# Kernel tuning notes

Measured on AMD Instinct MI355X. Metric: run time of the kernel, lower is better.

The kernel has to match this reference:

```python
import jax, jax.numpy as jnp
import numpy as np

B, DM, H, M, K = 2, 256, 4, 4096, 16
DIM = DM // H  # per-head feature dim = 64


def _proj(x, W, b):
    # 1x1 Conv2d on channels-first (B, C, M, K): pointwise linear over channels
    return jnp.einsum('oi,bimk->bomk', W, x) + b[None, :, None, None]


def setup_inputs() -> dict:
    rng = jax.random.key(0)
    ks = jax.random.split(rng, 11)
    s = 1.0 / np.sqrt(DM)
    return {
        'query': jax.random.normal(ks[0], (B, DM, M, 1), jnp.float32),
        'key':   jax.random.normal(ks[1], (B, DM, M, K), jnp.float32),
        'value': jax.random.normal(ks[2], (B, DM, M, K), jnp.float32),
        'Wq': jax.random.normal(ks[3], (DM, DM), jnp.float32) * s,
        'bq': jax.random.normal(ks[4], (DM,), jnp.float32) * 0.01,
        'Wk': jax.random.normal(ks[5], (DM, DM), jnp.float32) * s,
        'bk': jax.random.normal(ks[6], (DM,), jnp.float32) * 0.01,
        'Wv': jax.random.normal(ks[7], (DM, DM), jnp.float32) * s,
        'bv': jax.random.normal(ks[8], (DM,), jnp.float32) * 0.01,
        'Wm': jax.random.normal(ks[9], (DM, DM), jnp.float32) * s,
        'bm': jax.random.normal(ks[10], (DM,), jnp.float32) * 0.01,
    }


def reference(query, key, value, Wq, bq, Wk, bk, Wv, bv, Wm, bm):
    # project; torch view(B, dim, heads, -1) on channels-first => channel c -> (d=c//H, h=c%H)
    q = _proj(query, Wq, bq).reshape(B, DIM, H, M)          # (b, d, h, m)
    k = _proj(key,   Wk, bk).reshape(B, DIM, H, M, K)        # (b, d, h, m, k)
    v = _proj(value, Wv, bv).reshape(B, DIM, H, M, K)
    scores = jnp.einsum('bfhm,bfhmk->bhmk', q, k) / np.sqrt(DIM).astype(np.float32)
    prob = jax.nn.softmax(scores, axis=-1)                   # softmax over kn neighbors
    x = jnp.einsum('bhmk,bdhmk->bdhm', prob, v)              # (b, d, h, m)
    out = _proj(x.reshape(B, DM, M, 1), Wm, bm)              # merge 1x1 conv
    prob_sum = jnp.sum(prob, axis=1)                         # (b, m, k)
    return out, prob_sum
```

## Files before the change

kernel.cpp:

```cpp
#include <hip/hip_runtime.h>
#include <stdint.h>

#define DM_ 256
#define H_ 4
#define M_ 4096
#define KN_ 16
#define B_ 2
#define MK_ (M_*KN_)

typedef __attribute__((ext_vector_type(8))) short short8;
typedef __attribute__((ext_vector_type(4))) float f32x4;
typedef __attribute__((ext_vector_type(4))) unsigned short u16x4;

static __device__ __forceinline__ unsigned short f2bf(float x) {
  union { float f; uint32_t u; } v; v.f = x;
  uint32_t u = v.u + (0x7FFFu + ((v.u >> 16) & 1u));
  return (unsigned short)(u >> 16);
}
static __device__ __forceinline__ float u2f(uint32_t u) {
  union { uint32_t u; float f; } v; v.u = u; return v.f;
}

static __device__ __forceinline__ int swz512(int col, int kbyte) {
  int f = ((col >> 2) & 7) ^ ((col & 1) << 2);
  return (col << 9) + (kbyte ^ (f << 4));
}

__global__ void prep2(const float* __restrict__ Wq, const float* __restrict__ bq,
                      const float* __restrict__ Wk, const float* __restrict__ Wv,
                      const float* __restrict__ bv, const float* __restrict__ Wm,
                      const float* __restrict__ bm,
                      unsigned short* __restrict__ W2T, unsigned short* __restrict__ Wmv,
                      float* __restrict__ qb2, float* __restrict__ btot) {
  int t = blockIdx.x * 512 + threadIdx.x;
  if (t < 262144) {
    int j = t & 7, lane = (t >> 3) & 63, rowblk = (t >> 9) & 63, kstep = t >> 15;
    int row = rowblk * 16 + (lane & 15);
    int k = kstep * 32 + (lane >> 4) * 8 + j;
    int h = row >> 8, c = row & 255;
    float v = 0.f;
#pragma unroll 8
    for (int d = 0; d < 64; ++d) v += Wq[(4 * d + h) * 256 + k] * Wk[(4 * d + h) * 256 + c];
    W2T[t] = f2bf(v);
  } else if (t < 524288) {
    int e = t - 262144;
    int j = e & 7, lane = (e >> 3) & 63, rowblk = (e >> 9) & 15, kstep = e >> 13;
    int o = rowblk * 16 + (lane & 15);
    int kidx = kstep * 32 + (lane >> 4) * 8 + j;
    int c = kidx >> 2, h = kidx & 3;
    float v = 0.f;
#pragma unroll 8
    for (int d = 0; d < 64; ++d) v += Wm[o * 256 + 4 * d + h] * Wv[(4 * d + h) * 256 + c];
    Wmv[e] = f2bf(v);
  } else if (t < 525312) {
    int r = t - 524288; int h = r >> 8, c = r & 255;
    float v = 0.f;
#pragma unroll 8
    for (int d = 0; d < 64; ++d) v += bq[4 * d + h] * Wk[(4 * d + h) * 256 + c];
    qb2[r] = v;
  } else if (t < 525568) {
    int o = t - 525312;
    float v = bm[o];
#pragma unroll 8
    for (int c2 = 0; c2 < 256; ++c2) v += Wm[o * 256 + c2] * bv[c2];
    btot[o] = v;
  }
}

__global__ __launch_bounds__(512)
void qw_gemm(const float* __restrict__ query, const unsigned short* __restrict__ W2T,
             const float* __restrict__ qb2, unsigned short* __restrict__ qWbuf) {
  __shared__ unsigned short Xl[32 * 256];
  const int tid = threadIdx.x;
  const int lane = tid & 63, wid = tid >> 6;
  const int wr = wid >> 1, wc = wid & 1;
  const int mt = blockIdx.x & 127;
  const int rt = (blockIdx.x >> 7) & 3;
  const int b = blockIdx.x >> 9;
  const int m0 = mt * 32;
  const float* Xb = query + (size_t)b * DM_ * M_ + m0;
  const int c4 = 4 * (tid & 7);
  const int ch0 = 4 * (tid >> 3);
  float4 f[4];
#pragma unroll
  for (int i = 0; i < 4; ++i) f[i] = *(const float4*)(Xb + (size_t)(ch0 + i) * M_ + c4);
#pragma unroll
  for (int j = 0; j < 4; ++j) {
    u16x4 u = { f2bf(((const float*)&f[0])[j]), f2bf(((const float*)&f[1])[j]),
                f2bf(((const float*)&f[2])[j]), f2bf(((const float*)&f[3])[j]) };
    *(u16x4*)((char*)Xl + swz512(c4 + j, 2 * ch0)) = u;
  }
  __syncthreads();
  f32x4 acc[4] = {};
  const int bcol = wc * 16 + (lane & 15);
  const int rdk = 16 * (lane >> 4);
  short8 a_cur[4], a_nxt[4];
#pragma unroll
  for (int fi = 0; fi < 4; ++fi)
    a_cur[fi] = *(const short8*)(W2T + (size_t)(((rt * 16 + wr * 4 + fi) * 64 + lane) * 8));
#pragma unroll
  for (int kgs = 0; kgs < 8; ++kgs) {
    if (kgs < 7) {
#pragma unroll
      for (int fi = 0; fi < 4; ++fi)
        a_nxt[fi] = *(const short8*)(W2T + (size_t)((((kgs + 1) * 64 + rt * 16 + wr * 4 + fi) * 64 + lane) * 8));
    }
    short8 bb = *(const short8*)((const char*)Xl + swz512(bcol, 64 * kgs + rdk));
#pragma unroll
    for (int fi = 0; fi < 4; ++fi)
      acc[fi] = __builtin_amdgcn_mfma_f32_16x16x32_bf16(a_cur[fi], bb, acc[fi], 0, 0, 0);
#pragma unroll
    for (int fi = 0; fi < 4; ++fi) a_cur[fi] = a_nxt[fi];
  }
#pragma unroll
  for (int fi = 0; fi < 4; ++fi) {
#pragma unroll
    for (int r = 0; r < 4; ++r) {
      const int rr = rt * 256 + wr * 64 + fi * 16 + (lane >> 4) * 4 + r;
      qWbuf[(size_t)(b * 1024 + rr) * M_ + m0 + bcol] = f2bf(acc[fi][r] + qb2[rr]);
    }
  }
}

__global__ __launch_bounds__(1024, 8)
void fused_attn(const float* __restrict__ key, const float* __restrict__ value,
                const unsigned short* __restrict__ qW, const unsigned short* __restrict__ Wmv,
                const float* __restrict__ btot, float* __restrict__ out,
                float* __restrict__ psum) {
  __shared__ float ldsA[16 * 64 * 17];
  __shared__ float ldsP[16 * 4 * 16];
  unsigned short* qsl = (unsigned short*)ldsA;
  const int tid = threadIdx.x;
  const int lane = tid & 63;
  const int w = tid >> 6;
  const int vb = (blockIdx.x & 7) * 64 + (blockIdx.x >> 3);
  const int b = vb >> 8;
  const int m0 = (vb & 255) * 16;
  {
    const int c = tid & 255, h = tid >> 8;
    const unsigned short* src = qW + ((size_t)(b * 1024 + h * 256 + c)) * M_ + m0;
    uint4 rv[2];
    rv[0] = *(const uint4*)(src);
    rv[1] = *(const uint4*)(src + 8);
    const unsigned short* rs = (const unsigned short*)rv;
#pragma unroll
    for (int q = 0; q < 16; ++q) {
      const int slot = (q + c) & 15;
      qsl[c * 64 + slot * 4 + h] = rs[q];
    }
  }
  __syncthreads();
  const int mp = lane >> 2;
  const int kkq = lane & 3;
  const size_t cbase = (size_t)(b * 256) * 65536 + (size_t)m0 * 16 + lane * 4;
  f32x4 ps0 = {}, ps1 = {}, ps2 = {}, ps3 = {};
#pragma unroll 4
  for (int i = 0; i < 16; ++i) {
    const int c = i * 16 + w;
    const f32x4 kv = *(const f32x4*)(key + cbase + (size_t)c * 65536);
    const int slot = (mp + c) & 15;
    const uint2 qv = *(const uint2*)&qsl[c * 64 + slot * 4];
    ps0 += kv * u2f(qv.x << 16);
    ps1 += kv * u2f(qv.x & 0xffff0000u);
    ps2 += kv * u2f(qv.y << 16);
    ps3 += kv * u2f(qv.y & 0xffff0000u);
  }
  __syncthreads();
  {
    float* scx = ldsA + w * 1088 + lane * 17;
#pragma unroll
    for (int j = 0; j < 4; ++j) {
      scx[j]      = ps0[j];
      scx[4 + j]  = ps1[j];
      scx[8 + j]  = ps2[j];
      scx[12 + j] = ps3[j];
    }
  }
  __syncthreads();
  {
    const int mp2 = tid >> 6;
    const int h2 = (lane >> 4) & 3;
    const int kk = lane & 15;
    const int lanep = mp2 * 4 + (kk >> 2);
    const int idx = h2 * 4 + (kk & 3);
    float sc = 0.f;
#pragma unroll
    for (int w2 = 0; w2 < 16; ++w2) sc += ldsA[w2 * 1088 + lanep * 17 + idx];
    sc *= 0.125f;
    float mx = sc;
    mx = fmaxf(mx, __shfl_xor(mx, 1)); mx = fmaxf(mx, __shfl_xor(mx, 2));
    mx = fmaxf(mx, __shfl_xor(mx, 4)); mx = fmaxf(mx, __shfl_xor(mx, 8));
    const float e = __expf(sc - mx);
    float sm = e;
    sm += __shfl_xor(sm, 1); sm += __shfl_xor(sm, 2);
    sm += __shfl_xor(sm, 4); sm += __shfl_xor(sm, 8);
    const float pb = e / sm;
    ldsP[(mp2 * 4 + h2) * 16 + kk] = pb;
    float tot = pb;
    tot += __shfl_xor(tot, 16); tot += __shfl_xor(tot, 32);
    if (lane < 16)
      psum[((size_t)b * M_ + m0 + mp2) * KN_ + kk] = tot;
  }
  __syncthreads();
  {
    const f32x4 pr0 = *(const f32x4*)&ldsP[(mp * 4 + 0) * 16 + kkq * 4];
    const f32x4 pr1 = *(const f32x4*)&ldsP[(mp * 4 + 1) * 16 + kkq * 4];
    const f32x4 pr2 = *(const f32x4*)&ldsP[(mp * 4 + 2) * 16 + kkq * 4];
    const f32x4 pr3 = *(const f32x4*)&ldsP[(mp * 4 + 3) * 16 + kkq * 4];
#pragma unroll 4
    for (int i = 0; i < 16; ++i) {
      const int c = i * 16 + w;
      const f32x4 vv = *(const f32x4*)(value + cbase + (size_t)c * 65536);
      float p0 = pr0[0] * vv[0] + pr0[1] * vv[1] + pr0[2] * vv[2] + pr0[3] * vv[3];
      float p1 = pr1[0] * vv[0] + pr1[1] * vv[1] + pr1[2] * vv[2] + pr1[3] * vv[3];
      float p2 = pr2[0] * vv[0] + pr2[1] * vv[1] + pr2[2] * vv[2] + pr2[3] * vv[3];
      float p3 = pr3[0] * vv[0] + pr3[1] * vv[1] + pr3[2] * vv[2] + pr3[3] * vv[3];
      p0 += __shfl_xor(p0, 1); p0 += __shfl_xor(p0, 2);
      p1 += __shfl_xor(p1, 1); p1 += __shfl_xor(p1, 2);
      p2 += __shfl_xor(p2, 1); p2 += __shfl_xor(p2, 2);
      p3 += __shfl_xor(p3, 1); p3 += __shfl_xor(p3, 2);
      if (kkq == 0) {
        uint2 o;
        o.x = (uint32_t)f2bf(p0) | ((uint32_t)f2bf(p1) << 16);
        o.y = (uint32_t)f2bf(p2) | ((uint32_t)f2bf(p3) << 16);
        *(uint2*)((char*)ldsA + ((mp * 2048 + c * 8) ^ ((mp & 7) << 4))) = o;
      }
    }
  }
  __syncthreads();
  {
    const int wid = tid >> 6;
    const int bcol = lane & 15;
    const int kgrp = lane >> 4;
    f32x4 acc = {};
    for (int kgs = 0; kgs < 32; ++kgs) {
      const int byte = (bcol * 2048 + kgs * 64 + kgrp * 16) ^ ((bcol & 7) << 4);
      const short8 bb = *(const short8*)((const char*)ldsA + byte);
      const short8 a0 = *(const short8*)(Wmv + (size_t)(((kgs * 16 + wid) * 64 + lane) * 8));
      acc = __builtin_amdgcn_mfma_f32_16x16x32_bf16(a0, bb, acc, 0, 0, 0);
    }
#pragma unroll
    for (int r = 0; r < 4; ++r) {
      const int o = wid * 16 + kgrp * 4 + r;
      out[((size_t)(b * DM_ + o)) * M_ + m0 + bcol] = acc[r] + btot[o];
    }
  }
}

extern "C" void kernel_launch(void* const* d_in, const int* in_sizes, int n_in,
                              void* d_out, int out_size, void* d_ws, size_t ws_size,
                              hipStream_t stream) {
  const float* query = (const float*)d_in[0];
  const float* key   = (const float*)d_in[1];
  const float* value = (const float*)d_in[2];
  const float* Wq = (const float*)d_in[3];
  const float* bq = (const float*)d_in[4];
  const float* Wk = (const float*)d_in[5];
  const float* bk = (const float*)d_in[6];  (void)bk;
  const float* Wv = (const float*)d_in[7];
  const float* bv = (const float*)d_in[8];
  const float* Wm = (const float*)d_in[9];
  const float* bm = (const float*)d_in[10];
  float* out  = (float*)d_out;
  float* psum = out + (size_t)B_ * DM_ * M_;

  const size_t Wmv_off  = 524288;
  const size_t qb2_off  = 1048576;
  const size_t btot_off = 1052672;
  const size_t qW_off   = 1053696;

  unsigned short* W2T   = (unsigned short*)d_ws;
  unsigned short* Wmv   = (unsigned short*)((char*)d_ws + Wmv_off);
  float* qb2            = (float*)((char*)d_ws + qb2_off);
  float* btot           = (float*)((char*)d_ws + btot_off);
  unsigned short* qWbuf = (unsigned short*)((char*)d_ws + qW_off);

  prep2<<<dim3(1027), dim3(512), 0, stream>>>(Wq, bq, Wk, Wv, bv, Wm, bm, W2T, Wmv, qb2, btot);
  qw_gemm<<<dim3(B_ * 4 * 128), dim3(512), 0, stream>>>(query, W2T, qb2, qWbuf);
  fused_attn<<<dim3(512), dim3(1024), 0, stream>>>(key, value, qWbuf, Wmv, btot, out, psum);
}
```

Before: 103.3 us.

## Double-buffer key/value streaming via async global-to-LDS loads

Replaces direct per-thread global loads of key and value with global_load_lds DMA into a double-buffered LDS staging area. Each loop step issues the next 32-channel chunk before computing on the current one, with explicit vmcnt waits and barriers. The aim is to overlap memory latency with score and PV compute. The cost is a 100KB LDS footprint, which limits the kernel to one 1024-thread block per CU, plus extra block-wide barriers in every iteration.

```diff
diff --git a/kernel.cpp b/kernel.cpp
--- a/kernel.cpp
+++ b/kernel.cpp
@@ -122,14 +122,15 @@
   }
 }
 
-__global__ __launch_bounds__(1024, 8)
+__global__ __launch_bounds__(1024, 4)
 void fused_attn(const float* __restrict__ key, const float* __restrict__ value,
                 const unsigned short* __restrict__ qW, const unsigned short* __restrict__ Wmv,
                 const float* __restrict__ btot, float* __restrict__ out,
                 float* __restrict__ psum) {
-  __shared__ float ldsA[16 * 64 * 17];
-  __shared__ float ldsP[16 * 4 * 16];
-  unsigned short* qsl = (unsigned short*)ldsA;
+  __shared__ __align__(16) char LDS[102400];
+  unsigned short* qsl = (unsigned short*)(LDS + 65536);
+  float* scxp = (float*)LDS;
+  float* ldsP = (float*)(LDS + 98304);
   const int tid = threadIdx.x;
   const int lane = tid & 63;
   const int w = tid >> 6;
@@ -152,22 +153,54 @@
   __syncthreads();
   const int mp = lane >> 2;
   const int kkq = lane & 3;
-  const size_t cbase = (size_t)(b * 256) * 65536 + (size_t)m0 * 16 + lane * 4;
+  const float* ksrc = key   + (size_t)(b * 256) * 65536 + (size_t)m0 * 16 + lane * 4;
+  const float* vsrc = value + (size_t)(b * 256) * 65536 + (size_t)m0 * 16 + lane * 4;
+  auto issue2 = [&](const float* src, int i) {
+    const int h = i & 1;
+#pragma unroll
+    for (int j = 0; j < 2; ++j) {
+      const int r = w * 2 + j;
+      __builtin_amdgcn_global_load_lds(
+          (const __attribute__((address_space(1))) uint32_t*)(src + (size_t)(i * 32 + r) * 65536),
+          (__attribute__((address_space(3))) uint32_t*)(LDS + h * 32768 + r * 1024),
+          16, 0, 0);
+    }
+  };
   f32x4 ps0 = {}, ps1 = {}, ps2 = {}, ps3 = {};
-#pragma unroll 4
-  for (int i = 0; i < 16; ++i) {
-    const int c = i * 16 + w;
-    const f32x4 kv = *(const f32x4*)(key + cbase + (size_t)c * 65536);
-    const int slot = (mp + c) & 15;
-    const uint2 qv = *(const uint2*)&qsl[c * 64 + slot * 4];
-    ps0 += kv * u2f(qv.x << 16);
-    ps1 += kv * u2f(qv.x & 0xffff0000u);
-    ps2 += kv * u2f(qv.y << 16);
-    ps3 += kv * u2f(qv.y & 0xffff0000u);
-  }
+  auto scoreChunk = [&](int i) {
+    const int h = i & 1;
+#pragma unroll
+    for (int j = 0; j < 2; ++j) {
+      const int r = w * 2 + j;
+      const int c = i * 32 + r;
+      const f32x4 kv = *(const f32x4*)(LDS + h * 32768 + r * 1024 + lane * 16);
+      const int slot = (mp + c) & 15;
+      const uint2 qv = *(const uint2*)&qsl[c * 64 + slot * 4];
+      ps0 += kv * u2f(qv.x << 16);
+      ps1 += kv * u2f(qv.x & 0xffff0000u);
+      ps2 += kv * u2f(qv.y << 16);
+      ps3 += kv * u2f(qv.y & 0xffff0000u);
+    }
+  };
+  issue2(ksrc, 0);
+#pragma unroll 1
+  for (int i = 0; i < 7; ++i) {
+    issue2(ksrc, i + 1);
+    __builtin_amdgcn_sched_barrier(0);
+    asm volatile("s_waitcnt vmcnt(2)" ::: "memory");
+    __builtin_amdgcn_sched_barrier(0);
+    __builtin_amdgcn_s_barrier();
+    scoreChunk(i);
+    __builtin_amdgcn_s_barrier();
+    asm volatile("" ::: "memory");
+  }
+  asm volatile("s_waitcnt vmcnt(0)" ::: "memory");
+  __builtin_amdgcn_sched_barrier(0);
+  __builtin_amdgcn_s_barrier();
+  scoreChunk(7);
   __syncthreads();
   {
-    float* scx = ldsA + w * 1088 + lane * 17;
+    float* scx = scxp + w * 1088 + lane * 17;
 #pragma unroll
     for (int j = 0; j < 4; ++j) {
       scx[j]      = ps0[j];
@@ -185,7 +218,7 @@
     const int idx = h2 * 4 + (kk & 3);
     float sc = 0.f;
 #pragma unroll
-    for (int w2 = 0; w2 < 16; ++w2) sc += ldsA[w2 * 1088 + lanep * 17 + idx];
+    for (int w2 = 0; w2 < 16; ++w2) sc += scxp[w2 * 1088 + lanep * 17 + idx];
     sc *= 0.125f;
     float mx = sc;
     mx = fmaxf(mx, __shfl_xor(mx, 1)); mx = fmaxf(mx, __shfl_xor(mx, 2));
@@ -202,15 +235,17 @@
       psum[((size_t)b * M_ + m0 + mp2) * KN_ + kk] = tot;
   }
   __syncthreads();
-  {
-    const f32x4 pr0 = *(const f32x4*)&ldsP[(mp * 4 + 0) * 16 + kkq * 4];
-    const f32x4 pr1 = *(const f32x4*)&ldsP[(mp * 4 + 1) * 16 + kkq * 4];
-    const f32x4 pr2 = *(const f32x4*)&ldsP[(mp * 4 + 2) * 16 + kkq * 4];
-    const f32x4 pr3 = *(const f32x4*)&ldsP[(mp * 4 + 3) * 16 + kkq * 4];
-#pragma unroll 4
-    for (int i = 0; i < 16; ++i) {
-      const int c = i * 16 + w;
-      const f32x4 vv = *(const f32x4*)(value + cbase + (size_t)c * 65536);
+  const f32x4 pr0 = *(const f32x4*)&ldsP[(mp * 4 + 0) * 16 + kkq * 4];
+  const f32x4 pr1 = *(const f32x4*)&ldsP[(mp * 4 + 1) * 16 + kkq * 4];
+  const f32x4 pr2 = *(const f32x4*)&ldsP[(mp * 4 + 2) * 16 + kkq * 4];
+  const f32x4 pr3 = *(const f32x4*)&ldsP[(mp * 4 + 3) * 16 + kkq * 4];
+  auto pvChunk = [&](int i) {
+    const int h = i & 1;
+#pragma unroll
+    for (int j = 0; j < 2; ++j) {
+      const int r = w * 2 + j;
+      const int c = i * 32 + r;
+      const f32x4 vv = *(const f32x4*)(LDS + h * 32768 + r * 1024 + lane * 16);
       float p0 = pr0[0] * vv[0] + pr0[1] * vv[1] + pr0[2] * vv[2] + pr0[3] * vv[3];
       float p1 = pr1[0] * vv[0] + pr1[1] * vv[1] + pr1[2] * vv[2] + pr1[3] * vv[3];
       float p2 = pr2[0] * vv[0] + pr2[1] * vv[1] + pr2[2] * vv[2] + pr2[3] * vv[3];
@@ -223,10 +258,26 @@
         uint2 o;
         o.x = (uint32_t)f2bf(p0) | ((uint32_t)f2bf(p1) << 16);
         o.y = (uint32_t)f2bf(p2) | ((uint32_t)f2bf(p3) << 16);
-        *(uint2*)((char*)ldsA + ((mp * 2048 + c * 8) ^ ((mp & 7) << 4))) = o;
+        *(uint2*)(LDS + 65536 + ((mp * 2048 + c * 8) ^ ((mp & 7) << 4))) = o;
       }
     }
-  }
+  };
+  issue2(vsrc, 0);
+#pragma unroll 1
+  for (int i = 0; i < 7; ++i) {
+    issue2(vsrc, i + 1);
+    __builtin_amdgcn_sched_barrier(0);
+    asm volatile("s_waitcnt vmcnt(2)" ::: "memory");
+    __builtin_amdgcn_sched_barrier(0);
+    __builtin_amdgcn_s_barrier();
+    pvChunk(i);
+    __builtin_amdgcn_s_barrier();
+    asm volatile("" ::: "memory");
+  }
+  asm volatile("s_waitcnt vmcnt(0)" ::: "memory");
+  __builtin_amdgcn_sched_barrier(0);
+  __builtin_amdgcn_s_barrier();
+  pvChunk(7);
   __syncthreads();
   {
     const int wid = tid >> 6;
@@ -234,8 +285,8 @@
     const int kgrp = lane >> 4;
     f32x4 acc = {};
     for (int kgs = 0; kgs < 32; ++kgs) {
-      const int byte = (bcol * 2048 + kgs * 64 + kgrp * 16) ^ ((bcol & 7) << 4);
-      const short8 bb = *(const short8*)((const char*)ldsA + byte);
+      const int byte = 65536 + (((bcol * 2048 + kgs * 64 + kgrp * 16)) ^ ((bcol & 7) << 4));
+      const short8 bb = *(const short8*)(LDS + byte);
       const short8 a0 = *(const short8*)(Wmv + (size_t)(((kgs * 16 + wid) * 64 + lane) * 8));
       acc = __builtin_amdgcn_mfma_f32_16x16x32_bf16(a0, bb, acc, 0, 0, 0);
     }
```

Measured after the change: 112.4 us. 8.8% more time.

## Stream key/value through LDS rings with async global_load_lds prefetch

Applied to the files above, without the earlier changes.

Replaces the direct global reads of key and value with a three-slot per-wave LDS ring filled by global_load_lds. Progress is tracked with explicit vmcnt waits, and the first value chunks are issued before the softmax so their fetch overlaps it. Each wave now walks a contiguous range of channels, and the score scratch uses an XOR swizzle instead of padding. The prob-sum write moves to the end of the kernel. The aim is to hide memory latency in this bandwidth-bound kernel, but the LDS footprint grows to about 132 KB, which likely allows only one 1024-thread block per CU instead of two.

```diff
diff --git a/kernel.cpp b/kernel.cpp
--- a/kernel.cpp
+++ b/kernel.cpp
@@ -122,14 +122,15 @@
   }
 }
 
-__global__ __launch_bounds__(1024, 8)
+__global__ __launch_bounds__(1024, 4)
 void fused_attn(const float* __restrict__ key, const float* __restrict__ value,
                 const unsigned short* __restrict__ qW, const unsigned short* __restrict__ Wmv,
                 const float* __restrict__ btot, float* __restrict__ out,
                 float* __restrict__ psum) {
-  __shared__ float ldsA[16 * 64 * 17];
-  __shared__ float ldsP[16 * 4 * 16];
-  unsigned short* qsl = (unsigned short*)ldsA;
+  __shared__ __align__(16) char LDS[135168];
+  const int KRING = 0, QSL = 49152, SCX = 0, PVT = 49152, VRING = 81920, PROB = 131072;
+  unsigned short* qsl = (unsigned short*)(LDS + QSL);
+  float* ldsP = (float*)(LDS + PROB);
   const int tid = threadIdx.x;
   const int lane = tid & 63;
   const int w = tid >> 6;
@@ -152,40 +153,68 @@
   __syncthreads();
   const int mp = lane >> 2;
   const int kkq = lane & 3;
-  const size_t cbase = (size_t)(b * 256) * 65536 + (size_t)m0 * 16 + lane * 4;
+  const float* ksrc = key   + (size_t)(b * 256) * 65536 + (size_t)m0 * 16 + lane * 4;
+  const float* vsrc = value + (size_t)(b * 256) * 65536 + (size_t)m0 * 16 + lane * 4;
   f32x4 ps0 = {}, ps1 = {}, ps2 = {}, ps3 = {};
-#pragma unroll 4
-  for (int i = 0; i < 16; ++i) {
-    const int c = i * 16 + w;
-    const f32x4 kv = *(const f32x4*)(key + cbase + (size_t)c * 65536);
-    const int slot = (mp + c) & 15;
-    const uint2 qv = *(const uint2*)&qsl[c * 64 + slot * 4];
-    ps0 += kv * u2f(qv.x << 16);
-    ps1 += kv * u2f(qv.x & 0xffff0000u);
-    ps2 += kv * u2f(qv.y << 16);
-    ps3 += kv * u2f(qv.y & 0xffff0000u);
-  }
-  __syncthreads();
+
+#define KISS(ch, slot) \
+  __builtin_amdgcn_global_load_lds( \
+      (const __attribute__((address_space(1))) uint32_t*)(ksrc + (size_t)(w * 16 + (ch)) * 65536), \
+      (__attribute__((address_space(3))) uint32_t*)(LDS + KRING + w * 3072 + (slot) * 1024), 16, 0, 0)
+#define VISS(ch, slot) \
+  __builtin_amdgcn_global_load_lds( \
+      (const __attribute__((address_space(1))) uint32_t*)(vsrc + (size_t)(w * 16 + (ch)) * 65536), \
+      (__attribute__((address_space(3))) uint32_t*)(LDS + VRING + w * 3072 + (slot) * 1024), 16, 0, 0)
+#define KCONS(i, slot, n) { \
+    asm volatile("s_waitcnt vmcnt(" #n ")" ::: "memory"); \
+    __builtin_amdgcn_sched_barrier(0); \
+    const int c = w * 16 + (i); \
+    const f32x4 kv = *(const f32x4*)(LDS + KRING + w * 3072 + (slot) * 1024 + lane * 16); \
+    const uint2 qv = *(const uint2*)&qsl[c * 64 + (((mp + c) & 15)) * 4]; \
+    ps0 += kv * u2f(qv.x << 16); \
+    ps1 += kv * u2f(qv.x & 0xffff0000u); \
+    ps2 += kv * u2f(qv.y << 16); \
+    ps3 += kv * u2f(qv.y & 0xffff0000u); \
+  }
+  KISS(0, 0); KISS(1, 1); KISS(2, 2);
+  KCONS(0, 0, 2)  KISS(3, 0);
+  KCONS(1, 1, 2)  KISS(4, 1);
+  KCONS(2, 2, 2)  KISS(5, 2);
+  KCONS(3, 0, 2)  KISS(6, 0);
+  KCONS(4, 1, 2)  KISS(7, 1);
+  KCONS(5, 2, 2)  KISS(8, 2);
+  KCONS(6, 0, 2)  KISS(9, 0);
+  KCONS(7, 1, 2)  KISS(10, 1);
+  KCONS(8, 2, 2)  KISS(11, 2);
+  KCONS(9, 0, 2)  KISS(12, 0);
+  KCONS(10, 1, 2) KISS(13, 1);
+  KCONS(11, 2, 2) KISS(14, 2);
+  KCONS(12, 0, 2) KISS(15, 0);
+  KCONS(13, 1, 2)
+  KCONS(14, 2, 1)
+  KCONS(15, 0, 0)
+  VISS(0, 0); VISS(1, 1); VISS(2, 2);
+  __builtin_amdgcn_s_barrier();
   {
-    float* scx = ldsA + w * 1088 + lane * 17;
-#pragma unroll
-    for (int j = 0; j < 4; ++j) {
-      scx[j]      = ps0[j];
-      scx[4 + j]  = ps1[j];
-      scx[8 + j]  = ps2[j];
-      scx[12 + j] = ps3[j];
-    }
-  }
-  __syncthreads();
+    char* base = LDS + SCX + w * 4096 + lane * 64;
+    const int sw = (lane >> 1) & 3;
+    *(f32x4*)(base + ((0 ^ sw) << 4)) = ps0;
+    *(f32x4*)(base + ((1 ^ sw) << 4)) = ps1;
+    *(f32x4*)(base + ((2 ^ sw) << 4)) = ps2;
+    *(f32x4*)(base + ((3 ^ sw) << 4)) = ps3;
+  }
+  asm volatile("s_waitcnt lgkmcnt(0)" ::: "memory");
+  __builtin_amdgcn_s_barrier();
   {
     const int mp2 = tid >> 6;
     const int h2 = (lane >> 4) & 3;
     const int kk = lane & 15;
     const int lanep = mp2 * 4 + (kk >> 2);
-    const int idx = h2 * 4 + (kk & 3);
+    const int slotr = h2 ^ ((lanep >> 1) & 3);
+    const int off = SCX + lanep * 64 + (slotr << 4) + (kk & 3) * 4;
     float sc = 0.f;
 #pragma unroll
-    for (int w2 = 0; w2 < 16; ++w2) sc += ldsA[w2 * 1088 + lanep * 17 + idx];
+    for (int w2 = 0; w2 < 16; ++w2) sc += *(const float*)(LDS + w2 * 4096 + off);
     sc *= 0.125f;
     float mx = sc;
     mx = fmaxf(mx, __shfl_xor(mx, 1)); mx = fmaxf(mx, __shfl_xor(mx, 2));
@@ -194,48 +223,60 @@
     float sm = e;
     sm += __shfl_xor(sm, 1); sm += __shfl_xor(sm, 2);
     sm += __shfl_xor(sm, 4); sm += __shfl_xor(sm, 8);
-    const float pb = e / sm;
-    ldsP[(mp2 * 4 + h2) * 16 + kk] = pb;
-    float tot = pb;
-    tot += __shfl_xor(tot, 16); tot += __shfl_xor(tot, 32);
-    if (lane < 16)
-      psum[((size_t)b * M_ + m0 + mp2) * KN_ + kk] = tot;
-  }
-  __syncthreads();
-  {
-    const f32x4 pr0 = *(const f32x4*)&ldsP[(mp * 4 + 0) * 16 + kkq * 4];
-    const f32x4 pr1 = *(const f32x4*)&ldsP[(mp * 4 + 1) * 16 + kkq * 4];
-    const f32x4 pr2 = *(const f32x4*)&ldsP[(mp * 4 + 2) * 16 + kkq * 4];
-    const f32x4 pr3 = *(const f32x4*)&ldsP[(mp * 4 + 3) * 16 + kkq * 4];
-#pragma unroll 4
-    for (int i = 0; i < 16; ++i) {
-      const int c = i * 16 + w;
-      const f32x4 vv = *(const f32x4*)(value + cbase + (size_t)c * 65536);
-      float p0 = pr0[0] * vv[0] + pr0[1] * vv[1] + pr0[2] * vv[2] + pr0[3] * vv[3];
-      float p1 = pr1[0] * vv[0] + pr1[1] * vv[1] + pr1[2] * vv[2] + pr1[3] * vv[3];
-      float p2 = pr2[0] * vv[0] + pr2[1] * vv[1] + pr2[2] * vv[2] + pr2[3] * vv[3];
-      float p3 = pr3[0] * vv[0] + pr3[1] * vv[1] + pr3[2] * vv[2] + pr3[3] * vv[3];
-      p0 += __shfl_xor(p0, 1); p0 += __shfl_xor(p0, 2);
-      p1 += __shfl_xor(p1, 1); p1 += __shfl_xor(p1, 2);
-      p2 += __shfl_xor(p2, 1); p2 += __shfl_xor(p2, 2);
-      p3 += __shfl_xor(p3, 1); p3 += __shfl_xor(p3, 2);
-      if (kkq == 0) {
-        uint2 o;
-        o.x = (uint32_t)f2bf(p0) | ((uint32_t)f2bf(p1) << 16);
-        o.y = (uint32_t)f2bf(p2) | ((uint32_t)f2bf(p3) << 16);
-        *(uint2*)((char*)ldsA + ((mp * 2048 + c * 8) ^ ((mp & 7) << 4))) = o;
-      }
-    }
-  }
-  __syncthreads();
+    ldsP[(mp2 * 4 + h2) * 16 + kk] = e / sm;
+  }
+  asm volatile("s_waitcnt lgkmcnt(0)" ::: "memory");
+  __builtin_amdgcn_s_barrier();
+  const f32x4 pr0 = *(const f32x4*)&ldsP[(mp * 4 + 0) * 16 + kkq * 4];
+  const f32x4 pr1 = *(const f32x4*)&ldsP[(mp * 4 + 1) * 16 + kkq * 4];
+  const f32x4 pr2 = *(const f32x4*)&ldsP[(mp * 4 + 2) * 16 + kkq * 4];
+  const f32x4 pr3 = *(const f32x4*)&ldsP[(mp * 4 + 3) * 16 + kkq * 4];
+#define VCONS(i, slot, n) { \
+    asm volatile("s_waitcnt vmcnt(" #n ")" ::: "memory"); \
+    __builtin_amdgcn_sched_barrier(0); \
+    const int c = w * 16 + (i); \
+    const f32x4 vv = *(const f32x4*)(LDS + VRING + w * 3072 + (slot) * 1024 + lane * 16); \
+    float p0 = pr0[0] * vv[0] + pr0[1] * vv[1] + pr0[2] * vv[2] + pr0[3] * vv[3]; \
+    float p1 = pr1[0] * vv[0] + pr1[1] * vv[1] + pr1[2] * vv[2] + pr1[3] * vv[3]; \
+    float p2 = pr2[0] * vv[0] + pr2[1] * vv[1] + pr2[2] * vv[2] + pr2[3] * vv[3]; \
+    float p3 = pr3[0] * vv[0] + pr3[1] * vv[1] + pr3[2] * vv[2] + pr3[3] * vv[3]; \
+    p0 += __shfl_xor(p0, 1); p0 += __shfl_xor(p0, 2); \
+    p1 += __shfl_xor(p1, 1); p1 += __shfl_xor(p1, 2); \
+    p2 += __shfl_xor(p2, 1); p2 += __shfl_xor(p2, 2); \
+    p3 += __shfl_xor(p3, 1); p3 += __shfl_xor(p3, 2); \
+    if (kkq == 0) { \
+      uint2 o; \
+      o.x = (uint32_t)f2bf(p0) | ((uint32_t)f2bf(p1) << 16); \
+      o.y = (uint32_t)f2bf(p2) | ((uint32_t)f2bf(p3) << 16); \
+      *(uint2*)(LDS + PVT + ((mp * 2048 + c * 8) ^ ((mp & 7) << 4))) = o; \
+    } \
+  }
+  VCONS(0, 0, 2)  VISS(3, 0);
+  VCONS(1, 1, 2)  VISS(4, 1);
+  VCONS(2, 2, 2)  VISS(5, 2);
+  VCONS(3, 0, 2)  VISS(6, 0);
+  VCONS(4, 1, 2)  VISS(7, 1);
+  VCONS(5, 2, 2)  VISS(8, 2);
+  VCONS(6, 0, 2)  VISS(9, 0);
+  VCONS(7, 1, 2)  VISS(10, 1);
+  VCONS(8, 2, 2)  VISS(11, 2);
+  VCONS(9, 0, 2)  VISS(12, 0);
+  VCONS(10, 1, 2) VISS(13, 1);
+  VCONS(11, 2, 2) VISS(14, 2);
+  VCONS(12, 0, 2) VISS(15, 0);
+  VCONS(13, 1, 2)
+  VCONS(14, 2, 1)
+  VCONS(15, 0, 0)
+  asm volatile("s_waitcnt lgkmcnt(0)" ::: "memory");
+  __builtin_amdgcn_s_barrier();
   {
     const int wid = tid >> 6;
     const int bcol = lane & 15;
     const int kgrp = lane >> 4;
     f32x4 acc = {};
     for (int kgs = 0; kgs < 32; ++kgs) {
-      const int byte = (bcol * 2048 + kgs * 64 + kgrp * 16) ^ ((bcol & 7) << 4);
-      const short8 bb = *(const short8*)((const char*)ldsA + byte);
+      const int byte = PVT + (((bcol * 2048 + kgs * 64 + kgrp * 16)) ^ ((bcol & 7) << 4));
+      const short8 bb = *(const short8*)(LDS + byte);
       const short8 a0 = *(const short8*)(Wmv + (size_t)(((kgs * 16 + wid) * 64 + lane) * 8));
       acc = __builtin_amdgcn_mfma_f32_16x16x32_bf16(a0, bb, acc, 0, 0, 0);
     }
@@ -245,6 +286,16 @@
       out[((size_t)(b * DM_ + o)) * M_ + m0 + bcol] = acc[r] + btot[o];
     }
   }
+  if (tid < 256) {
+    const int mp2 = tid >> 4, kk = tid & 15;
+    psum[((size_t)b * M_ + m0 + mp2) * KN_ + kk] =
+        ldsP[(mp2 * 4 + 0) * 16 + kk] + ldsP[(mp2 * 4 + 1) * 16 + kk] +
+        ldsP[(mp2 * 4 + 2) * 16 + kk] + ldsP[(mp2 * 4 + 3) * 16 + kk];
+  }
+#undef KISS
+#undef VISS
+#undef KCONS
+#undef VCONS
 }
 
 extern "C" void kernel_launch(void* const* d_in, const int* in_sizes, int n_in,
```

After: 109.2 us. +5.7%, slower.
